# Optimization experiments

Measured on AMD Instinct MI355X. Metric: run time of the kernel, lower is better.

The kernel has to match this reference:

```python
import math
import jax, jax.numpy as jnp
import numpy as np
from jax import lax

B, C, H, W, D = 8, 3, 512, 512, 256
KS, SIGMA = 13, 2.0  # GaussianBlur(13); torchvision samples sigma in (0.1,5.0) -> fixed for determinism


def tanh01(v):
    return jnp.tanh(v) * 0.5 + 0.5


def tanh_range(v, left, right):
    return tanh01(v) * (right - left) + left


def norm01(v):
    return (v - v.min()) / (v.max() - v.min())


def gaussian_blur(x):
    r = KS // 2
    t = jnp.arange(KS, dtype=x.dtype) - r
    k = jnp.exp(-(t ** 2) / (2.0 * SIGMA ** 2))
    k = k / k.sum()
    b, c, h, w = x.shape
    xp = jnp.pad(x, ((0, 0), (0, 0), (r, r), (r, r)), mode='reflect').reshape(b * c, 1, h + 2 * r, w + 2 * r)
    y = lax.conv_general_dilated(xp, k.reshape(1, 1, KS, 1), (1, 1), 'VALID')
    y = lax.conv_general_dilated(y, k.reshape(1, 1, 1, KS), (1, 1), 'VALID')
    return y.reshape(b, c, h, w)


def dark_channel(x):
    return x.min(axis=1, keepdims=True)


def atmospheric_light(x, dark, top_k=1000):
    b, _, h, w = x.shape
    imsz = h * w
    numpx = max(imsz // top_k, 1)
    darkvec = dark.reshape(b, imsz)
    imvec = x.reshape(b, 3, imsz).transpose(0, 2, 1)  # [b, imsz, 3]
    idx = jnp.argsort(darkvec, axis=1)[:, imsz - numpx:]  # brightest dark-channel pixels
    gathered = jnp.take_along_axis(imvec, idx[:, :, None], axis=1)  # [b, numpx, 3]
    a = gathered[:, 1:, :].sum(axis=1) / numpx  # original loop skips index 0 of the slice
    return a[:, :, None, None]  # [b,3,1,1]


def fft_filter(x, rate, fft_gate):
    # rate: [b,1]; replicate torch.fft.fftshift default (shifts ALL axes, incl. batch/channel)
    b, c, w, h = x.shape  # note: original names w,h = shape[-2:]
    line = jnp.floor(jnp.sqrt(w * h * rate) / 2.0).astype(jnp.int32).reshape(-1)  # [b]
    rows = jnp.arange(w)
    cols = jnp.arange(h)
    mr = (rows[None, :] >= w // 2 - line[:, None]) & (rows[None, :] < w // 2 + line[:, None])
    mc = (cols[None, :] >= h // 2 - line[:, None]) & (cols[None, :] < h // 2 + line[:, None])
    mask = (mr[:, None, :, None] & mc[:, None, None, :]).astype(x.dtype)  # [b,1,w,h]
    mask = jnp.broadcast_to(mask, x.shape)
    F = jnp.fft.fftshift(jnp.fft.fft2(x, norm='forward'))
    F = F * (1.0 - mask)
    inv = jnp.fft.ifft2(jnp.fft.ifftshift(F), norm='forward').real
    return jnp.abs(inv) * fft_gate[:, None, None, None]


def setup_inputs() -> dict:
    key = jax.random.key(0)
    ks = jax.random.split(key, 20)
    def lin_w(k, i, o):
        return (jax.random.normal(k, (i, o)) * 0.02).astype(jnp.float32)
    def lin_b(k, o):
        return (jax.random.normal(k, (o,)) * 0.02).astype(jnp.float32)
    return {
        'x': jax.random.uniform(ks[0], (B, C, H, W), dtype=jnp.float32),
        'latent': (jax.random.normal(ks[1], (B, D)) * 0.5).astype(jnp.float32),
        'gate_w': lin_w(ks[2], D, 8), 'gate_b': lin_b(ks[3], 8),
        'wb_w': lin_w(ks[4], D, 3), 'wb_b': lin_b(ks[5], 3),
        'gamma_w': lin_w(ks[6], D, 1), 'gamma_b': lin_b(ks[7], 1),
        'sharp_w': lin_w(ks[8], D, 1), 'sharp_b': lin_b(ks[9], 1),
        'defog_w': lin_w(ks[10], D, 1), 'defog_b': lin_b(ks[11], 1),
        'contrast_w': lin_w(ks[12], D, 1), 'contrast_b': lin_b(ks[13], 1),
        'tone_w': lin_w(ks[14], D, 8), 'tone_b': lin_b(ks[15], 8),
        'fft_w': lin_w(ks[16], D, 1), 'fft_b': lin_b(ks[17], 1),
    }


def reference(x, latent, gate_w, gate_b, wb_w, wb_b, gamma_w, gamma_b, sharp_w, sharp_b,
              defog_w, defog_b, contrast_w, contrast_b, tone_w, tone_b, fft_w, fft_b):
    gate = tanh_range(latent @ gate_w + gate_b, 0.01, 1.0)  # [B,8]

    # white balance
    wb = jnp.exp(tanh_range(latent @ wb_w + wb_b, -0.5, 0.5))
    cs = 1.0 / (1e-5 + 0.27 * wb[:, 0] + 0.67 * wb[:, 1] + 0.06 * wb[:, 2])
    wb = cs[:, None] * wb
    wb_out = norm01(wb[:, :, None, None] * x) * gate[:, 0][:, None, None, None]

    # gamma balance
    lg = math.log(2.5)
    gamma = jnp.exp(tanh_range(latent @ gamma_w + gamma_b, -lg, lg))[:, :, None, None]
    g_out = norm01(jnp.maximum(x, 1e-4) ** gamma) * gate[:, 1][:, None, None, None]

    # identity
    id_out = x * gate[:, 2][:, None, None, None]

    # sharpening
    y = tanh_range(latent @ sharp_w + sharp_b, 0.1, 1.0)[:, :, None, None]
    s = x + y * (x - gaussian_blur(x))
    sharp_out = norm01(s) * gate[:, 3][:, None, None, None]

    # defog (atmospheric scattering model)
    omega = tanh_range(latent @ defog_w + defog_b, 0.1, 1.0)[:, :, None, None]
    dark = dark_channel(x)
    a = atmospheric_light(x, dark)
    t = 1.0 - omega * dark_channel(x / a)
    j = (x - a) / jnp.maximum(t, 0.01) + a
    fog_out = norm01(j) * gate[:, 4][:, None, None, None]

    # contrast
    alpha = jnp.tanh(latent @ contrast_w + contrast_b)[:, :, None, None]
    lum = jnp.clip(0.27 * x[:, 0] + 0.67 * x[:, 1] + 0.06 * x[:, 2], 0.0, 1.0)[:, None]
    clum = -jnp.cos(math.pi * lum) * 0.5 + 0.5
    cimg = x / (lum + 1e-6) * clum
    cimg = (1.0 - alpha) * x + alpha * cimg
    contrast_out = norm01(cimg) * gate[:, 5][:, None, None, None]

    # tone curve (8 fixed segments)
    tc = tanh_range(latent @ tone_w + tone_b, 0.5, 2.0)  # [B,8]
    tsum = tc.sum(axis=1) + 1e-30
    total = jnp.zeros_like(x)
    for i in range(8):
        total = total + jnp.clip(x - i / 8.0, 0.0, 1.0 / 8.0) * tc[:, i][:, None, None, None]
    total = total * (8.0 / tsum)[:, None, None, None]
    tone_out = norm01(total) * gate[:, 6][:, None, None, None]

    # fft frequency masking
    rate = tanh_range(latent @ fft_w + fft_b, 0.1, 0.8)  # [B,1]
    fft_out = fft_filter(x, rate, gate[:, 7])

    return norm01(wb_out + g_out + id_out + sharp_out + fog_out + contrast_out + tone_out + fft_out)
```

## Files before the change

### kernel.cpp

```cpp
#include <hip/hip_runtime.h>
#include <math.h>

#define HW 262144
#define TOTAL 6291456
#define PI_F 3.14159265358979323846f
#define NBIN 1024
#define PIDX(i) ((i) + ((i) >> 3))


#define PF_GATE 0
#define PF_WB 64
#define PF_GAMMA 88
#define PF_Y 96
#define PF_OMEGA 104
#define PF_ALPHA 112
#define PF_TC 120
#define PF_TSC 184
#define PF_RATE 192
#define PF_FG 200
#define PF_A 208
#define PF_WBM 256
#define PF_WBA 264
#define PF_GM 272
#define PF_GA 280
#define PF_SM 288
#define PF_SA 296
#define PF_FM 304
#define PF_FA 312
#define PF_CM 320
#define PF_CA 328
#define PF_TM 336
#define PF_TA 344
#define PF_LINE 360
#define PF_TCS 368
#define PF_TPRE 432
#define PF_IA 496

#define QX(b,c) ((b)*3+(c))
#define QS 24
#define QJ 25
#define QC 26
#define QFIN 27
#define SL_LCOUNT 1792
#define SL_BINSTAR 1920
#define SL_RNEED 1928
#define SL_SUMA2 2048

struct GK { float w[13]; };

__device__ __forceinline__ void waveFence(){ __builtin_amdgcn_wave_barrier(); }

__device__ __forceinline__ unsigned fkey(float f){
    unsigned u = __float_as_uint(f);
    return (u & 0x80000000u) ? ~u : (u | 0x80000000u);
}
__device__ __forceinline__ float funkey(unsigned k){
    return (k & 0x80000000u) ? __uint_as_float(k & 0x7FFFFFFFu) : __uint_as_float(~k);
}

__device__ __forceinline__ void blockRedPair(unsigned kmn, unsigned kmx, int q,
                                             unsigned* slots, unsigned* lds8){
    #pragma unroll
    for (int o = 32; o > 0; o >>= 1){
        kmn = min(kmn, __shfl_down(kmn, o));
        kmx = max(kmx, __shfl_down(kmx, o));
    }
    int w = threadIdx.x >> 6;
    if ((threadIdx.x & 63) == 0){ lds8[w] = kmn; lds8[4+w] = kmx; }
    __syncthreads();
    if (threadIdx.x == 0){
        unsigned mn = min(min(lds8[0],lds8[1]), min(lds8[2],lds8[3]));
        unsigned mx = max(max(lds8[4],lds8[5]), max(lds8[6],lds8[7]));
        int s = blockIdx.x & 31;
        atomicMin(&slots[q*64 + s], mn);
        atomicMax(&slots[q*64 + 32 + s], mx);
    }
    __syncthreads();
}

__device__ __forceinline__ float toneF(float v, const float* tc, float tsc){
    float tn = 0.f;
    #pragma unroll
    for (int i = 0; i < 8; ++i){
        float d = v - 0.125f * (float)i;
        d = fminf(fmaxf(d, 0.f), 0.125f);
        tn += d * tc[i];
    }
    return tn * tsc;
}

__device__ __forceinline__ float2 cadd(float2 a, float2 b){ return make_float2(a.x+b.x, a.y+b.y); }
__device__ __forceinline__ float2 csub(float2 a, float2 b){ return make_float2(a.x-b.x, a.y-b.y); }
__device__ __forceinline__ float2 cmul(float2 a, float2 b){ return make_float2(a.x*b.x - a.y*b.y, a.x*b.y + a.y*b.x); }

template<int S>
__device__ __forceinline__ float2 rot90(float2 z){
    return (S < 0) ? make_float2(z.y, -z.x) : make_float2(-z.y, z.x);
}

template<int S>
__device__ __forceinline__ void fft4p(float2 a, float2 b, float2 c, float2 d,
                                      float2& X0, float2& X1, float2& X2, float2& X3){
    float2 t0 = cadd(a,c), t1 = csub(a,c), t2 = cadd(b,d), t3 = csub(b,d);
    float2 it3 = rot90<S>(t3);
    X0 = cadd(t0,t2); X2 = csub(t0,t2);
    X1 = cadd(t1,it3); X3 = csub(t1,it3);
}

template<int S>
__device__ __forceinline__ void bfly8(float2 v[8]){
    const float C = 0.70710678118654752f;
    float2 E0,E1,E2,E3,O0,O1,O2,O3;
    fft4p<S>(v[0],v[2],v[4],v[6], E0,E1,E2,E3);
    fft4p<S>(v[1],v[3],v[5],v[7], O0,O1,O2,O3);
    float2 w1 = make_float2(C, (S<0) ? -C : C);
    float2 w3 = make_float2(-C, (S<0) ? -C : C);
    float2 u1 = cmul(O1, w1);
    float2 u2 = rot90<S>(O2);
    float2 u3 = cmul(O3, w3);
    v[0]=cadd(E0,O0); v[4]=csub(E0,O0);
    v[1]=cadd(E1,u1); v[5]=csub(E1,u1);
    v[2]=cadd(E2,u2); v[6]=csub(E2,u2);
    v[3]=cadd(E3,u3); v[7]=csub(E3,u3);
}

__device__ __forceinline__ void twiddles(float2 v[8], float th){
    float sn, cs; __sincosf(th, &sn, &cs);
    float2 w1 = make_float2(cs, sn);
    float2 w = w1;
    v[1] = cmul(v[1], w1);
    #pragma unroll
    for (int r = 2; r < 8; ++r){ w = cmul(w, w1); v[r] = cmul(v[r], w); }
}

template<int S>
__device__ __forceinline__ void fft512reg(float2 v[8], float2* buf, int lane){
    bfly8<S>(v);
    #pragma unroll
    for (int q = 0; q < 8; ++q) buf[PIDX(8*lane + q)] = v[q];
    waveFence();
    #pragma unroll
    for (int r = 0; r < 8; ++r) v[r] = buf[PIDX(lane + 64*r)];
    waveFence();
    twiddles(v, (float)S * 6.2831853072f * (float)(lane & 7) * (1.0f/64.0f));
    bfly8<S>(v);
    {
        int basei = ((lane >> 3) << 6) + (lane & 7);
        #pragma unroll
        for (int q = 0; q < 8; ++q) buf[PIDX(basei + 8*q)] = v[q];
    }
    waveFence();
    #pragma unroll
    for (int r = 0; r < 8; ++r) v[r] = buf[PIDX(lane + 64*r)];
    waveFence();
    twiddles(v, (float)S * 6.2831853072f * (float)lane * (1.0f/512.0f));
    bfly8<S>(v);
}

__global__ __launch_bounds__(256) void kSetup(
    const float* __restrict__ lat,
    const float* gw, const float* gb, const float* wbw, const float* wbb,
    const float* gaw, const float* gab, const float* shw, const float* shb,
    const float* dfw, const float* dfb, const float* ctw, const float* ctb,
    const float* tow, const float* tob, const float* ffw, const float* ffb,
    float* P, unsigned* slots, unsigned* hist)
{
    if (blockIdx.x != 0){
        int i = (blockIdx.x - 1) * 256 + threadIdx.x;
        if (i < 4096) slots[i] = (i < 1792 && (i & 63) < 32) ? 0xFFFFFFFFu : 0u;
        if (i < 8192) hist[i] = 0u;
        return;
    }
    int t = threadIdx.x;
    if (t < 192){
        int b = t / 24, o = t % 24;
        const float* L = lat + b * 256;
        const float* W; float bias; int nc, col;
        if (o < 8)      { W=gw;  bias=gb[o];     nc=8; col=o;    }
        else if (o < 11){ W=wbw; bias=wbb[o-8];  nc=3; col=o-8;  }
        else if (o==11) { W=gaw; bias=gab[0];    nc=1; col=0;    }
        else if (o==12) { W=shw; bias=shb[0];    nc=1; col=0;    }
        else if (o==13) { W=dfw; bias=dfb[0];    nc=1; col=0;    }
        else if (o==14) { W=ctw; bias=ctb[0];    nc=1; col=0;    }
        else if (o<23)  { W=tow; bias=tob[o-15]; nc=8; col=o-15; }
        else            { W=ffw; bias=ffb[0];    nc=1; col=0;    }
        float acc = bias;
        for (int d = 0; d < 256; ++d) acc += L[d] * W[d*nc + col];
        float t01 = tanhf(acc) * 0.5f + 0.5f;
        if (o < 8){ float v = t01*0.99f + 0.01f; P[PF_GATE + b*8 + o] = v; if (o==7) P[PF_FG + b] = v; }
        else if (o < 11){ P[PF_WB + b*3 + (o-8)] = expf(t01 - 0.5f); }
        else if (o==11){ float lg = logf(2.5f); P[PF_GAMMA + b] = expf(t01*(2.f*lg) - lg); }
        else if (o==12){ P[PF_Y + b] = t01*0.9f + 0.1f; }
        else if (o==13){ P[PF_OMEGA + b] = t01*0.9f + 0.1f; }
        else if (o==14){ P[PF_ALPHA + b] = tanhf(acc); }
        else if (o<23){ P[PF_TC + b*8 + (o-15)] = t01*1.5f + 0.5f; }
        else { P[PF_RATE + b] = t01*0.7f + 0.1f; }
    }
    __syncthreads();
    if (t < 8){
        int b = t;
        float w0=P[PF_WB+b*3], w1=P[PF_WB+b*3+1], w2=P[PF_WB+b*3+2];
        float cs = 1.0f / (1e-5f + 0.27f*w0 + 0.67f*w1 + 0.06f*w2);
        P[PF_WB+b*3] = cs*w0; P[PF_WB+b*3+1] = cs*w1; P[PF_WB+b*3+2] = cs*w2;
        float ts = 0.f;
        for (int i = 0; i < 8; ++i) ts += P[PF_TC + b*8 + i];
        float tsc = 8.0f / (ts + 1e-30f);
        P[PF_TSC + b] = tsc;
        float acc = 0.f;
        for (int k = 0; k < 8; ++k){
            float tck = P[PF_TC + b*8 + k] * tsc;
            P[PF_TCS + b*8 + k] = tck;
            P[PF_TPRE + b*8 + k] = acc;
            acc += tck * 0.125f;
        }
        int bs = (b + 4) & 7;
        ((int*)(P + PF_LINE))[b] = (int)floorf(sqrtf(262144.0f * P[PF_RATE + bs]) * 0.5f);
    }
}

__global__ __launch_bounds__(256) void kMinmaxHist(const float* __restrict__ x, unsigned* slots, unsigned* hist){
    __shared__ unsigned h[NBIN];
    __shared__ unsigned lds8[8];
    int b = blockIdx.x >> 7;
    int blk = blockIdx.x & 127;
    for (int i = threadIdx.x; i < NBIN; i += 256) h[i] = 0u;
    __syncthreads();
    size_t xb = (size_t)b*3*HW;
    int p0 = (((blk<<1)    )*256 + threadIdx.x) << 2;
    int p1 = (((blk<<1) + 1)*256 + threadIdx.x) << 2;
    float4 u0 = *(const float4*)(x + xb + p0);
    float4 u1 = *(const float4*)(x + xb + HW + p0);
    float4 u2 = *(const float4*)(x + xb + 2*HW + p0);
    float4 w0 = *(const float4*)(x + xb + p1);
    float4 w1 = *(const float4*)(x + xb + HW + p1);
    float4 w2 = *(const float4*)(x + xb + 2*HW + p1);
    float a0[8] = {u0.x,u0.y,u0.z,u0.w, w0.x,w0.y,w0.z,w0.w};
    float a1[8] = {u1.x,u1.y,u1.z,u1.w, w1.x,w1.y,w1.z,w1.w};
    float a2[8] = {u2.x,u2.y,u2.z,u2.w, w2.x,w2.y,w2.z,w2.w};
    float mn0=1e30f,mx0=-1e30f,mn1=1e30f,mx1=-1e30f,mn2=1e30f,mx2=-1e30f;
    #pragma unroll
    for (int e = 0; e < 8; ++e){
        float dark = fminf(a0[e], fminf(a1[e], a2[e]));
        atomicAdd(&h[min(NBIN-1, (int)(dark * (float)NBIN))], 1u);
        mn0 = fminf(mn0, a0[e]); mx0 = fmaxf(mx0, a0[e]);
        mn1 = fminf(mn1, a1[e]); mx1 = fmaxf(mx1, a1[e]);
        mn2 = fminf(mn2, a2[e]); mx2 = fmaxf(mx2, a2[e]);
    }
    __syncthreads();
    for (int i = threadIdx.x; i < NBIN; i += 256){
        unsigned c = h[i];
        if (c) atomicAdd(&hist[b*NBIN + i], c);
    }
    blockRedPair(fkey(mn0), fkey(mx0), QX(b,0), slots, lds8);
    blockRedPair(fkey(mn1), fkey(mx1), QX(b,1), slots, lds8);
    blockRedPair(fkey(mn2), fkey(mx2), QX(b,2), slots, lds8);
}

__global__ __launch_bounds__(256) void kScanHist(const unsigned* __restrict__ hist, unsigned* slots){
    int b = blockIdx.x, t = threadIdx.x;
    __shared__ unsigned wtot[4];
    __shared__ int doneS;
    if (t == 0) doneS = 0;
    __syncthreads();
    unsigned total = 0;
    for (int c0 = 0; c0 < NBIN; c0 += 256){
        int binIdx = NBIN-1 - (c0 + t);
        unsigned cnt = hist[b*NBIN + binIdx];
        unsigned v = cnt;
        #pragma unroll
        for (int off = 1; off < 64; off <<= 1){
            unsigned u = __shfl_up(v, off);
            if ((t & 63) >= off) v += u;
        }
        if ((t & 63) == 63) wtot[t >> 6] = v;
        __syncthreads();
        unsigned wofs = 0;
        for (int w = 0; w < (t >> 6); ++w) wofs += wtot[w];
        unsigned incl = total + wofs + v;
        unsigned excl = incl - cnt;
        if (incl >= 261u && excl < 261u){
            slots[SL_BINSTAR + b] = (unsigned)binIdx;
            slots[SL_RNEED + b]   = 261u - excl;
            doneS = 1;
        }
        __syncthreads();
        if (doneS) break;
        total += wtot[0] + wtot[1] + wtot[2] + wtot[3];
        __syncthreads();
    }
}

__global__ __launch_bounds__(256) void kCollect(const float* __restrict__ x, unsigned* slots, uint2* list){
    __shared__ float wsum[3][4];
    int b = blockIdx.x >> 8;
    int tile = blockIdx.x & 255;
    size_t xb = (size_t)b*3*HW;
    int p = (tile*256 + threadIdx.x) << 2;
    float4 v0 = *(const float4*)(x + xb + p);
    float4 v1 = *(const float4*)(x + xb + HW + p);
    float4 v2 = *(const float4*)(x + xb + 2*HW + p);
    int bs = (int)slots[SL_BINSTAR + b];
    float a0[4] = {v0.x,v0.y,v0.z,v0.w};
    float a1[4] = {v1.x,v1.y,v1.z,v1.w};
    float a2[4] = {v2.x,v2.y,v2.z,v2.w};
    float s0 = 0.f, s1 = 0.f, s2 = 0.f;
    #pragma unroll
    for (int e = 0; e < 4; ++e){
        float dark = fminf(a0[e], fminf(a1[e], a2[e]));
        int bin = min(NBIN-1, (int)(dark * (float)NBIN));
        if (bin > bs){ s0 += a0[e]; s1 += a1[e]; s2 += a2[e]; }
        else if (bin == bs){
            unsigned n = atomicAdd(&slots[SL_LCOUNT + b], 1u);
            if (n < 1024u) list[(b << 10) + n] = make_uint2(__float_as_uint(dark), (unsigned)(p + e));
        }
    }
    #pragma unroll
    for (int o = 32; o > 0; o >>= 1){
        s0 += __shfl_down(s0, o); s1 += __shfl_down(s1, o); s2 += __shfl_down(s2, o);
    }
    int w = threadIdx.x >> 6;
    if ((threadIdx.x & 63) == 0){ wsum[0][w] = s0; wsum[1][w] = s1; wsum[2][w] = s2; }
    __syncthreads();
    if (threadIdx.x == 0){
        float t0 = wsum[0][0]+wsum[0][1]+wsum[0][2]+wsum[0][3];
        float t1 = wsum[1][0]+wsum[1][1]+wsum[1][2]+wsum[1][3];
        float t2 = wsum[2][0]+wsum[2][1]+wsum[2][2]+wsum[2][3];
        float* F = (float*)(slots + SL_SUMA2);
        int sl = blockIdx.x & 31;
        atomicAdd(&F[(b*3+0)*32 + sl], t0);
        atomicAdd(&F[(b*3+1)*32 + sl], t1);
        atomicAdd(&F[(b*3+2)*32 + sl], t2);
    }
}

__global__ void kSelect(const float* __restrict__ x, uint2* list, unsigned* slots, float* P){
    __shared__ unsigned pid[262];
    __shared__ char taken[1024];
    int b = blockIdx.x, t = threadIdx.x;
    int n = (int)min(slots[SL_LCOUNT + b], 1024u);
    int r = (int)slots[SL_RNEED + b];
    if (r > n) r = n;
    const uint2* L = &list[b << 10];
    for (int i = t; i < n; i += 64) taken[i] = 0;
    __syncthreads();
    for (int it = 0; it < r; ++it){
        unsigned long long bk = 0ull; int bp = -1;
        for (int i = t; i < n; i += 64){
            if (taken[i]) continue;
            uint2 e = L[i];
            unsigned long long key = ((unsigned long long)e.x << 32) | e.y;
            if (key > bk){ bk = key; bp = i; }
        }
        #pragma unroll
        for (int o = 32; o > 0; o >>= 1){
            unsigned long long ok = __shfl_down(bk, o);
            int op = __shfl_down(bp, o);
            if (ok > bk){ bk = ok; bp = op; }
        }
        bp = __shfl(bp, 0);
        if (t == 0){ pid[it] = L[bp].y; taken[bp] = 1; }
        __syncthreads();
    }
    float s0 = 0.f, s1 = 0.f, s2 = 0.f;
    size_t xb = (size_t)b*3*HW;
    for (int i = t; i < r; i += 64){
        unsigned id = pid[i];
        s0 += x[xb + id]; s1 += x[xb + HW + id]; s2 += x[xb + 2*HW + id];
    }
    #pragma unroll
    for (int o = 32; o > 0; o >>= 1){
        s0 += __shfl_down(s0, o); s1 += __shfl_down(s1, o); s2 += __shfl_down(s2, o);
    }
    if (t == 0){
        const float* F = (const float*)(slots + SL_SUMA2);
        float f0 = 0.f, f1 = 0.f, f2 = 0.f;
        for (int k = 0; k < 32; ++k){
            f0 += F[(b*3+0)*32 + k];
            f1 += F[(b*3+1)*32 + k];
            f2 += F[(b*3+2)*32 + k];
        }
        float A0 = (s0 + f0) / 262.0f, A1 = (s1 + f1) / 262.0f, A2 = (s2 + f2) / 262.0f;
        P[PF_A + b*3+0] = A0; P[PF_A + b*3+1] = A1; P[PF_A + b*3+2] = A2;
        P[PF_IA + b*3+0] = 1.0f/A0; P[PF_IA + b*3+1] = 1.0f/A1; P[PF_IA + b*3+2] = 1.0f/A2;
    }
}

__global__ __launch_bounds__(256) void kBlur(const float* __restrict__ x, float* __restrict__ blurOut,
                                             const float* __restrict__ P, unsigned* slots, GK gk){
    __shared__ float tile[76][80];
    __shared__ float hbuf[76][68];
    __shared__ unsigned lds8[8];
    int img = blockIdx.x >> 6;
    int tid = blockIdx.x & 63;
    int tr0 = (tid >> 3) << 6;
    int tc0 = (tid & 7) << 6;
    size_t ib = (size_t)img * HW;
    int t = threadIdx.x;
    for (int l = t; l < 76*76; l += 256){
        int r = l / 76, c = l - r*76;
        int gr = tr0 + r - 6; gr = (gr < 0) ? -gr : ((gr > 511) ? 1022 - gr : gr);
        int gc = tc0 + c - 6; gc = (gc < 0) ? -gc : ((gc > 511) ? 1022 - gc : gc);
        tile[r][c] = x[ib + ((size_t)gr << 9) + gc];
    }
    __syncthreads();
    for (int l = t; l < 76*64; l += 256){
        int r = l >> 6, c = l & 63;
        float acc = 0.f;
        #pragma unroll
        for (int k = 0; k < 13; ++k) acc += gk.w[k] * tile[r][c + k];
        hbuf[r][c] = acc;
    }
    __syncthreads();
    float yb = P[PF_Y + img/3];
    unsigned kmn = 0xFFFFFFFFu, kmx = 0u;
    for (int l = t; l < 64*64; l += 256){
        int r = l >> 6, c = l & 63;
        float acc = 0.f;
        #pragma unroll
        for (int k = 0; k < 13; ++k) acc += gk.w[k] * hbuf[r + k][c];
        blurOut[ib + ((size_t)(tr0 + r) << 9) + tc0 + c] = acc;
        float xv = tile[r + 6][c + 6];
        float s = xv + yb * (xv - acc);
        unsigned key = fkey(s);
        kmn = min(kmn, key); kmx = max(kmx, key);
    }
    blockRedPair(kmn, kmx, QS, slots, lds8);
}

__global__ __launch_bounds__(256) void kFftRowFwdJC(const float* __restrict__ x, float2* __restrict__ bc,
                                                    const float* __restrict__ P, unsigned* slots){
    __shared__ float2 buf4[4][580];
    __shared__ unsigned lds8[8];
    float (*xs)[3][512] = reinterpret_cast<float(*)[3][512]>(&buf4[0][0]);
    int b = blockIdx.x >> 8;
    int rp = blockIdx.x & 255;
    int t = threadIdx.x;
    #pragma unroll
    for (int k = 0; k < 3; ++k){
        int l = t + (k << 8);
        int seg = l >> 7;
        int idx = (l & 127) << 2;
        int ch = seg >> 1, rr = seg & 1;
        float4 z = *(const float4*)(x + (size_t)(3*b + ch)*HW + ((size_t)(2*rp + rr) << 9) + idx);
        *(float4*)&xs[rr][ch][idx] = z;
    }
    __syncthreads();
    {
        float ia0 = P[PF_IA+b*3], ia1 = P[PF_IA+b*3+1], ia2 = P[PF_IA+b*3+2];
        float a0 = P[PF_A+b*3],  a1 = P[PF_A+b*3+1],  a2 = P[PF_A+b*3+2];
        float om = P[PF_OMEGA+b], al = P[PF_ALPHA+b];
        int rr = t >> 7, c4 = (t & 127) << 2;
        float4 xv0 = *(float4*)&xs[rr][0][c4];
        float4 xv1 = *(float4*)&xs[rr][1][c4];
        float4 xv2 = *(float4*)&xs[rr][2][c4];
        float A0[4]={xv0.x,xv0.y,xv0.z,xv0.w}, A1[4]={xv1.x,xv1.y,xv1.z,xv1.w}, A2[4]={xv2.x,xv2.y,xv2.z,xv2.w};
        float jmn = 1e30f, jmx = -1e30f, cmn = 1e30f, cmx = -1e30f;
        #pragma unroll
        for (int e = 0; e < 4; ++e){
            float x0 = A0[e], x1 = A1[e], x2 = A2[e];
            float dr = fminf(x0*ia0, fminf(x1*ia1, x2*ia2));
            float T = fmaxf(1.0f - om*dr, 0.01f);
            float rT = 1.0f / T;
            float j0 = (x0-a0)*rT + a0, j1 = (x1-a1)*rT + a1, j2 = (x2-a2)*rT + a2;
            float lum = fminf(fmaxf(0.27f*x0 + 0.67f*x1 + 0.06f*x2, 0.f), 1.f);
            float clum = -__cosf(PI_F*lum)*0.5f + 0.5f;
            float alx = (1.f - al) + al * (clum / (lum + 1e-6f));
            float c0 = x0*alx, c1 = x1*alx, c2 = x2*alx;
            jmn = fminf(jmn, fminf(j0, fminf(j1, j2))); jmx = fmaxf(jmx, fmaxf(j0, fmaxf(j1, j2)));
            cmn = fminf(cmn, fminf(c0, fminf(c1, c2))); cmx = fmaxf(cmx, fmaxf(c0, fmaxf(c1, c2)));
        }
        blockRedPair(fkey(jmn), fkey(jmx), QJ, slots, lds8);
        blockRedPair(fkey(cmn), fkey(cmx), QC, slots, lds8);
    }
    int u = t >> 6, lane = t & 63;
    int frr = u >> 1, pk = u & 1;
    float2 v[8];
    #pragma unroll
    for (int r = 0; r < 8; ++r){
        int i = lane + 64*r;
        if (pk == 0) v[r] = make_float2(xs[frr][0][i] * (1.0f/512.0f), xs[frr][1][i] * (1.0f/512.0f));
        else         v[r] = make_float2(xs[frr][2][i] * (1.0f/512.0f), 0.f);
    }
    __syncthreads();
    fft512reg<-1>(v, buf4[u], lane);
    size_t ob = (size_t)(2*b + pk)*HW + ((size_t)(2*rp + frr) << 9);
    #pragma unroll
    for (int q = 0; q < 8; ++q) bc[ob + lane + 64*q] = v[q];
}

__global__ __launch_bounds__(256) void kFftColMid(float2* __restrict__ bc, const int* __restrict__ lineS){
    int img  = blockIdx.x >> 6;
    int tile = blockIdx.x & 63;
    int c0 = tile << 3;
    int line = lineS[img >> 1];
    if (c0 >= line && c0 + 8 <= 512 - line) return;
    __shared__ float2 cb[8][580];
    int t = threadIdx.x;
    size_t ibase = (size_t)img*HW + c0;
    for (int k = 0; k < 16; ++k){
        int idx = (k << 8) + t;
        int row = idx >> 3, col = idx & 7;
        float2 z = bc[ibase + ((size_t)row << 9) + col];
        cb[col][PIDX(row)] = make_float2(z.x * (1.0f/512.0f), z.y * (1.0f/512.0f));
    }
    __syncthreads();
    int lane = t & 63, u = t >> 6;
    #pragma unroll
    for (int h = 0; h < 2; ++h){
        int col = (h << 2) + u;
        int cc = c0 + col;
        bool colM = (cc < line) || (cc >= 512 - line);
        float2 v[8];
        #pragma unroll
        for (int r = 0; r < 8; ++r) v[r] = cb[col][PIDX(lane + 64*r)];
        waveFence();
        fft512reg<-1>(v, cb[col], lane);
        if (colM){
            #pragma unroll
            for (int q = 0; q < 8; ++q){
                int f = lane + (q << 6);
                if (f < line || f >= 512 - line) v[q] = make_float2(0.f, 0.f);
            }
        }
        waveFence();
        fft512reg<+1>(v, cb[col], lane);
        #pragma unroll
        for (int q = 0; q < 8; ++q) cb[col][PIDX(lane + 64*q)] = v[q];
        waveFence();
    }
    __syncthreads();
    for (int k = 0; k < 16; ++k){
        int idx = (k << 8) + t;
        int row = idx >> 3, col = idx & 7;
        int cc = c0 + col;
        if (cc < line || cc >= 512 - line)
            bc[ibase + ((size_t)row << 9) + col] = cb[col][PIDX(row)];
    }
}

__global__ __launch_bounds__(256) void kCombineFFT(const float* __restrict__ x, float* __restrict__ outb,
                                                   const float2* __restrict__ bc, const float* __restrict__ P,
                                                   unsigned* slots){
    __shared__ float2 buf4[4][580];
    __shared__ float stc[8], spre[8];
    __shared__ unsigned lds8[8];
    float (*fbuf)[3][512] = reinterpret_cast<float(*)[3][512]>(&buf4[0][0]);
    int b = blockIdx.x >> 8;
    int rp = blockIdx.x & 255;
    int t = threadIdx.x;
    if (t < 8){ stc[t] = P[PF_TCS + b*8 + t]; spre[t] = P[PF_TPRE + b*8 + t]; }
    int u = t >> 6, lane = t & 63;
    int frr = u >> 1, pk = u & 1;
    float2 v[8];
    size_t ib = (size_t)(2*b + pk)*HW + ((size_t)(2*rp + frr) << 9);
    #pragma unroll
    for (int r = 0; r < 8; ++r) v[r] = bc[ib + lane + 64*r];
    fft512reg<+1>(v, buf4[u], lane);
    __syncthreads();
    if (pk == 0){
        #pragma unroll
        for (int q = 0; q < 8; ++q){
            int i = lane + 64*q;
            fbuf[frr][0][i] = fabsf(v[q].x);
            fbuf[frr][1][i] = fabsf(v[q].y);
        }
    } else {
        #pragma unroll
        for (int q = 0; q < 8; ++q) fbuf[frr][2][lane + 64*q] = fabsf(v[q].x);
    }
    __syncthreads();

    float g  = P[PF_FG + b];
    float wb0=P[PF_WB+b*3], wb1=P[PF_WB+b*3+1], wb2=P[PF_WB+b*3+2];
    float gam=P[PF_GAMMA+b], yb=P[PF_Y+b], om=P[PF_OMEGA+b], al=P[PF_ALPHA+b];
    float a0=P[PF_A+b*3], a1=P[PF_A+b*3+1], a2=P[PF_A+b*3+2];
    float ia0=P[PF_IA+b*3], ia1=P[PF_IA+b*3+1], ia2=P[PF_IA+b*3+2];
    float g2=P[PF_GATE+b*8+2];
    float wbm=P[PF_WBM+b], wba=P[PF_WBA+b], gm=P[PF_GM+b], ga=P[PF_GA+b];
    float sm=P[PF_SM+b], sa=P[PF_SA+b], fm=P[PF_FM+b], fa=P[PF_FA+b];
    float cm=P[PF_CM+b], ca=P[PF_CA+b], tm=P[PF_TM+b], ta=P[PF_TA+b];
    float kadd = wba + ga + sa + fa + ca + ta;

    int rr = t >> 7, c4 = (t & 127) << 2;
    size_t p0 = (size_t)(3*b)*HW + ((size_t)(2*rp + rr) << 9) + c4;
    float4 xv0 = *(const float4*)(x + p0);
    float4 xv1 = *(const float4*)(x + p0 + HW);
    float4 xv2 = *(const float4*)(x + p0 + 2*HW);
    float4 bv0 = *(const float4*)(outb + p0);
    float4 bv1 = *(const float4*)(outb + p0 + HW);
    float4 bv2 = *(const float4*)(outb + p0 + 2*HW);
    float4 fv0 = *(float4*)&fbuf[rr][0][c4];
    float4 fv1 = *(float4*)&fbuf[rr][1][c4];
    float4 fv2 = *(float4*)&fbuf[rr][2][c4];
    float X0[4]={xv0.x,xv0.y,xv0.z,xv0.w}, X1[4]={xv1.x,xv1.y,xv1.z,xv1.w}, X2[4]={xv2.x,xv2.y,xv2.z,xv2.w};
    float B0[4]={bv0.x,bv0.y,bv0.z,bv0.w}, B1[4]={bv1.x,bv1.y,bv1.z,bv1.w}, B2[4]={bv2.x,bv2.y,bv2.z,bv2.w};
    float F0[4]={fv0.x,fv0.y,fv0.z,fv0.w}, F1[4]={fv1.x,fv1.y,fv1.z,fv1.w}, F2[4]={fv2.x,fv2.y,fv2.z,fv2.w};
    float O0[4], O1[4], O2[4];
    float mn = 1e30f, mx = -1e30f;
    #pragma unroll
    for (int e = 0; e < 4; ++e){
        float x0 = X0[e], x1 = X1[e], x2 = X2[e];
        float dr = fminf(x0*ia0, fminf(x1*ia1, x2*ia2));
        float T = fmaxf(1.0f - om*dr, 0.01f);
        float rT = 1.0f / T;
        float lum = fminf(fmaxf(0.27f*x0 + 0.67f*x1 + 0.06f*x2, 0.f), 1.f);
        float clum = -__cosf(PI_F*lum)*0.5f + 0.5f;
        float alx = (1.f - al) + al * (clum / (lum + 1e-6f));
        #pragma unroll
        for (int ch = 0; ch < 3; ++ch){
            float xv = (ch==0)?x0:((ch==1)?x1:x2);
            float bl = (ch==0)?B0[e]:((ch==1)?B1[e]:B2[e]);
            float fv = (ch==0)?F0[e]:((ch==1)?F1[e]:F2[e]);
            float wb = (ch==0)?wb0:((ch==1)?wb1:wb2);
            float av = (ch==0)?a0:((ch==1)?a1:a2);
            float s = xv + yb*(xv - bl);
            float j = (xv - av)*rT + av;
            float ci = xv * alx;
            int k = min(7, (int)(xv * 8.0f));
            float tn = spre[k] + (xv - 0.125f*(float)k) * stc[k];
            float gp = __powf(fmaxf(xv, 1e-4f), gam);
            float sum = (wb*xv)*wbm + gp*gm + xv*g2 + s*sm + j*fm + ci*cm + tn*tm + kadd + fv*g;
            if (ch==0) O0[e]=sum; else if (ch==1) O1[e]=sum; else O2[e]=sum;
            mn = fminf(mn, sum); mx = fmaxf(mx, sum);
        }
    }
    *(float4*)(outb + p0)        = make_float4(O0[0],O0[1],O0[2],O0[3]);
    *(float4*)(outb + p0 + HW)   = make_float4(O1[0],O1[1],O1[2],O1[3]);
    *(float4*)(outb + p0 + 2*HW) = make_float4(O2[0],O2[1],O2[2],O2[3]);
    blockRedPair(fkey(mn), fkey(mx), QFIN, slots, lds8);
}

__global__ void kNormParams(float* P, const unsigned* __restrict__ slots){
    __shared__ float mnv[28], mxv[28];
    int t = threadIdx.x;
    if (t < 28){
        unsigned kmn = 0xFFFFFFFFu, kmx = 0u;
        for (int s = 0; s < 32; ++s){
            kmn = min(kmn, slots[t*64 + s]);
            kmx = max(kmx, slots[t*64 + 32 + s]);
        }
        mnv[t] = funkey(kmn); mxv[t] = funkey(kmx);
    }
    __syncthreads();
    if (t == 0){
        float wmin=1e30f, wmax=-1e30f, gmin=1e30f, gmax=-1e30f, tmin=1e30f, tmax=-1e30f;
        for (int b = 0; b < 8; ++b){
            float gam = P[PF_GAMMA+b];
            float tsc = P[PF_TSC+b];
            const float* tc = &P[PF_TC + b*8];
            float xbmin = 1e30f, xbmax = -1e30f;
            for (int c = 0; c < 3; ++c){
                int i = b*3 + c;
                float w = P[PF_WB + i];
                wmin = fminf(wmin, w * mnv[i]); wmax = fmaxf(wmax, w * mxv[i]);
                gmin = fminf(gmin, __powf(fmaxf(mnv[i], 1e-4f), gam));
                gmax = fmaxf(gmax, __powf(fmaxf(mxv[i], 1e-4f), gam));
                xbmin = fminf(xbmin, mnv[i]); xbmax = fmaxf(xbmax, mxv[i]);
            }
            tmin = fminf(tmin, toneF(xbmin, tc, tsc));
            tmax = fmaxf(tmax, toneF(xbmax, tc, tsc));
        }
        float smin = mnv[QS], smax = mxv[QS];
        float jmin = mnv[QJ], jmax = mxv[QJ];
        float cmin = mnv[QC], cmax = mxv[QC];
        for (int b = 0; b < 8; ++b){
            const float* G = &P[PF_GATE + b*8];
            float m;
            m = G[0]/(wmax-wmin); P[PF_WBM+b]=m; P[PF_WBA+b]=-wmin*m;
            m = G[1]/(gmax-gmin); P[PF_GM +b]=m; P[PF_GA +b]=-gmin*m;
            m = G[3]/(smax-smin); P[PF_SM +b]=m; P[PF_SA +b]=-smin*m;
            m = G[4]/(jmax-jmin); P[PF_FM +b]=m; P[PF_FA +b]=-jmin*m;
            m = G[5]/(cmax-cmin); P[PF_CM +b]=m; P[PF_CA +b]=-cmin*m;
            m = G[6]/(tmax-tmin); P[PF_TM +b]=m; P[PF_TA +b]=-tmin*m;
        }
    }
}

__global__ __launch_bounds__(256) void kFinalNorm(float* __restrict__ out, const unsigned* __restrict__ slots){
    unsigned kmn = 0xFFFFFFFFu, kmx = 0u;
    for (int s = 0; s < 32; ++s){
        kmn = min(kmn, slots[QFIN*64 + s]);
        kmx = max(kmx, slots[QFIN*64 + 32 + s]);
    }
    float mn = funkey(kmn), mx = funkey(kmx);
    float inv = 1.0f / (mx - mn);
    size_t i = ((size_t)blockIdx.x*256 + threadIdx.x) << 2;
    float4 v = *(const float4*)(out + i);
    v.x = (v.x - mn) * inv; v.y = (v.y - mn) * inv;
    v.z = (v.z - mn) * inv; v.w = (v.w - mn) * inv;
    *(float4*)(out + i) = v;
}

extern "C" void kernel_launch(void* const* d_in, const int* in_sizes, int n_in,
                              void* d_out, int out_size, void* d_ws, size_t ws_size,
                              hipStream_t stream){
    const float* x   = (const float*)d_in[0];
    const float* lat = (const float*)d_in[1];
    const float* gw  = (const float*)d_in[2];  const float* gb  = (const float*)d_in[3];
    const float* wbw = (const float*)d_in[4];  const float* wbb = (const float*)d_in[5];
    const float* gaw = (const float*)d_in[6];  const float* gab = (const float*)d_in[7];
    const float* shw = (const float*)d_in[8];  const float* shb = (const float*)d_in[9];
    const float* dfw = (const float*)d_in[10]; const float* dfb = (const float*)d_in[11];
    const float* ctw = (const float*)d_in[12]; const float* ctb = (const float*)d_in[13];
    const float* tow = (const float*)d_in[14]; const float* tob = (const float*)d_in[15];
    const float* ffw = (const float*)d_in[16]; const float* ffb = (const float*)d_in[17];
    float* out = (float*)d_out;
    char* ws = (char*)d_ws;

    float*    P     = (float*)ws;
    unsigned* slots = (unsigned*)(ws + 4096);
    unsigned* hist  = (unsigned*)(ws + 20480);
    uint2*    list  = (uint2*)(ws + 540672);
    float2*   bufC  = (float2*)(ws + 1048576);
    const int* lineS = (const int*)(P + PF_LINE);

    GK gk;
    {
        float s = 0.f;
        for (int i = 0; i < 13; ++i){ float t = (float)i - 6.f; gk.w[i] = expf(-(t*t)/8.0f); s += gk.w[i]; }
        for (int i = 0; i < 13; ++i) gk.w[i] /= s;
    }

    hipLaunchKernelGGL(kSetup,       dim3(41),   dim3(256), 0, stream, lat, gw,gb,wbw,wbb,gaw,gab,shw,shb,dfw,dfb,ctw,ctb,tow,tob,ffw,ffb, P, slots, hist);
    hipLaunchKernelGGL(kMinmaxHist,  dim3(1024), dim3(256), 0, stream, x, slots, hist);
    hipLaunchKernelGGL(kScanHist,    dim3(8),    dim3(256), 0, stream, hist, slots);
    hipLaunchKernelGGL(kCollect,     dim3(2048), dim3(256), 0, stream, x, slots, list);
    hipLaunchKernelGGL(kSelect,      dim3(8),    dim3(64),  0, stream, x, list, slots, P);
    hipLaunchKernelGGL(kBlur,        dim3(1536), dim3(256), 0, stream, x, out, P, slots, gk);
    hipLaunchKernelGGL(kFftRowFwdJC, dim3(2048), dim3(256), 0, stream, x, bufC, P, slots);
    hipLaunchKernelGGL(kFftColMid,   dim3(1024), dim3(256), 0, stream, bufC, lineS);
    hipLaunchKernelGGL(kNormParams,  dim3(1),    dim3(64),  0, stream, P, slots);
    hipLaunchKernelGGL(kCombineFFT,  dim3(2048), dim3(256), 0, stream, x, out, bufC, P, slots);
    hipLaunchKernelGGL(kFinalNorm,   dim3(6144), dim3(256), 0, stream, out, slots);
}
```

Measured before the change: 199.4 us.

## Pack two real channel-2 rows per complex FFT and split spectra after transform

The row FFT kernels now process four rows per block with six waves. Channels 0 and 1 are packed into one complex FFT per row, and channel 2 of two adjacent rows shares one complex FFT. The two real spectra are separated with the conjugate-symmetry trick, so five of the previous six 512-point FFTs per row pair's worth of work become fewer transforms. The inverse kernel recombines the channel-2 pair before a single inverse FFT. This adds an LDS round trip and a separation step, and changes the block shape to 384 threads with 1024 blocks.

Result: slower. 212.3 us (+6.5%).

```diff
diff --git a/kernel.cpp b/kernel.cpp
--- a/kernel.cpp
+++ b/kernel.cpp
@@ -58,19 +58,19 @@
     return (k & 0x80000000u) ? __uint_as_float(k & 0x7FFFFFFFu) : __uint_as_float(~k);
 }
 
-__device__ __forceinline__ void blockRedPair(unsigned kmn, unsigned kmx, int q,
-                                             unsigned* slots, unsigned* lds8){
+__device__ __forceinline__ void blockRedPairN(unsigned kmn, unsigned kmx, int q,
+                                              unsigned* slots, unsigned* ldsw, int nw){
     #pragma unroll
     for (int o = 32; o > 0; o >>= 1){
         kmn = min(kmn, __shfl_down(kmn, o));
         kmx = max(kmx, __shfl_down(kmx, o));
     }
     int w = threadIdx.x >> 6;
-    if ((threadIdx.x & 63) == 0){ lds8[w] = kmn; lds8[4+w] = kmx; }
+    if ((threadIdx.x & 63) == 0){ ldsw[w] = kmn; ldsw[nw + w] = kmx; }
     __syncthreads();
     if (threadIdx.x == 0){
-        unsigned mn = min(min(lds8[0],lds8[1]), min(lds8[2],lds8[3]));
-        unsigned mx = max(max(lds8[4],lds8[5]), max(lds8[6],lds8[7]));
+        unsigned mn = ldsw[0], mx = ldsw[nw];
+        for (int i = 1; i < nw; ++i){ mn = min(mn, ldsw[i]); mx = max(mx, ldsw[nw+i]); }
         int s = blockIdx.x & 31;
         atomicMin(&slots[q*64 + s], mn);
         atomicMax(&slots[q*64 + 32 + s], mx);
@@ -251,9 +251,9 @@
         unsigned c = h[i];
         if (c) atomicAdd(&hist[b*NBIN + i], c);
     }
-    blockRedPair(fkey(mn0), fkey(mx0), QX(b,0), slots, lds8);
-    blockRedPair(fkey(mn1), fkey(mx1), QX(b,1), slots, lds8);
-    blockRedPair(fkey(mn2), fkey(mx2), QX(b,2), slots, lds8);
+    blockRedPairN(fkey(mn0), fkey(mx0), QX(b,0), slots, lds8, 4);
+    blockRedPairN(fkey(mn1), fkey(mx1), QX(b,1), slots, lds8, 4);
+    blockRedPairN(fkey(mn2), fkey(mx2), QX(b,2), slots, lds8, 4);
 }
 
 __global__ __launch_bounds__(256) void kScanHist(const unsigned* __restrict__ hist, unsigned* slots){
@@ -424,68 +424,97 @@
         unsigned key = fkey(s);
         kmn = min(kmn, key); kmx = max(kmx, key);
     }
-    blockRedPair(kmn, kmx, QS, slots, lds8);
-}
-
-__global__ __launch_bounds__(256) void kFftRowFwdJC(const float* __restrict__ x, float2* __restrict__ bc,
+    blockRedPairN(kmn, kmx, QS, slots, lds8, 4);
+}
+
+__global__ __launch_bounds__(384) void kFftRowFwdJC(const float* __restrict__ x, float2* __restrict__ bc,
                                                     const float* __restrict__ P, unsigned* slots){
-    __shared__ float2 buf4[4][580];
-    __shared__ unsigned lds8[8];
-    float (*xs)[3][512] = reinterpret_cast<float(*)[3][512]>(&buf4[0][0]);
-    int b = blockIdx.x >> 8;
-    int rp = blockIdx.x & 255;
+    __shared__ float2 buf6[6][580];
+    __shared__ unsigned lds12[12];
+    float (*xs)[3][512] = reinterpret_cast<float(*)[3][512]>(&buf6[0][0]);
+    int b = blockIdx.x >> 7;
+    int rq = blockIdx.x & 127;
     int t = threadIdx.x;
     #pragma unroll
-    for (int k = 0; k < 3; ++k){
-        int l = t + (k << 8);
-        int seg = l >> 7;
+    for (int k = 0; k < 4; ++k){
+        int l = t + k*384;
+        int rc = l >> 7;
         int idx = (l & 127) << 2;
-        int ch = seg >> 1, rr = seg & 1;
-        float4 z = *(const float4*)(x + (size_t)(3*b + ch)*HW + ((size_t)(2*rp + rr) << 9) + idx);
-        *(float4*)&xs[rr][ch][idx] = z;
+        int row = rc / 3, ch = rc - row*3;
+        float4 z = *(const float4*)(x + (size_t)(3*b + ch)*HW + ((size_t)(4*rq + row) << 9) + idx);
+        *(float4*)&xs[row][ch][idx] = z;
     }
     __syncthreads();
     {
         float ia0 = P[PF_IA+b*3], ia1 = P[PF_IA+b*3+1], ia2 = P[PF_IA+b*3+2];
         float a0 = P[PF_A+b*3],  a1 = P[PF_A+b*3+1],  a2 = P[PF_A+b*3+2];
         float om = P[PF_OMEGA+b], al = P[PF_ALPHA+b];
-        int rr = t >> 7, c4 = (t & 127) << 2;
-        float4 xv0 = *(float4*)&xs[rr][0][c4];
-        float4 xv1 = *(float4*)&xs[rr][1][c4];
-        float4 xv2 = *(float4*)&xs[rr][2][c4];
-        float A0[4]={xv0.x,xv0.y,xv0.z,xv0.w}, A1[4]={xv1.x,xv1.y,xv1.z,xv1.w}, A2[4]={xv2.x,xv2.y,xv2.z,xv2.w};
         float jmn = 1e30f, jmx = -1e30f, cmn = 1e30f, cmx = -1e30f;
-        #pragma unroll
-        for (int e = 0; e < 4; ++e){
-            float x0 = A0[e], x1 = A1[e], x2 = A2[e];
-            float dr = fminf(x0*ia0, fminf(x1*ia1, x2*ia2));
-            float T = fmaxf(1.0f - om*dr, 0.01f);
-            float rT = 1.0f / T;
-            float j0 = (x0-a0)*rT + a0, j1 = (x1-a1)*rT + a1, j2 = (x2-a2)*rT + a2;
-            float lum = fminf(fmaxf(0.27f*x0 + 0.67f*x1 + 0.06f*x2, 0.f), 1.f);
-            float clum = -__cosf(PI_F*lum)*0.5f + 0.5f;
-            float alx = (1.f - al) + al * (clum / (lum + 1e-6f));
-            float c0 = x0*alx, c1 = x1*alx, c2 = x2*alx;
-            jmn = fminf(jmn, fminf(j0, fminf(j1, j2))); jmx = fmaxf(jmx, fmaxf(j0, fmaxf(j1, j2)));
-            cmn = fminf(cmn, fminf(c0, fminf(c1, c2))); cmx = fmaxf(cmx, fmaxf(c0, fmaxf(c1, c2)));
-        }
-        blockRedPair(fkey(jmn), fkey(jmx), QJ, slots, lds8);
-        blockRedPair(fkey(cmn), fkey(cmx), QC, slots, lds8);
+        for (int it = 0; it < 2; ++it){
+            int g = t + it*384;
+            if (g >= 512) break;
+            int row = g >> 7, c4 = (g & 127) << 2;
+            float4 xv0 = *(float4*)&xs[row][0][c4];
+            float4 xv1 = *(float4*)&xs[row][1][c4];
+            float4 xv2 = *(float4*)&xs[row][2][c4];
+            float A0[4]={xv0.x,xv0.y,xv0.z,xv0.w}, A1[4]={xv1.x,xv1.y,xv1.z,xv1.w}, A2[4]={xv2.x,xv2.y,xv2.z,xv2.w};
+            #pragma unroll
+            for (int e = 0; e < 4; ++e){
+                float x0 = A0[e], x1 = A1[e], x2 = A2[e];
+                float dr = fminf(x0*ia0, fminf(x1*ia1, x2*ia2));
+                float T = fmaxf(1.0f - om*dr, 0.01f);
+                float rT = 1.0f / T;
+                float j0 = (x0-a0)*rT + a0, j1 = (x1-a1)*rT + a1, j2 = (x2-a2)*rT + a2;
+                float lum = fminf(fmaxf(0.27f*x0 + 0.67f*x1 + 0.06f*x2, 0.f), 1.f);
+                float clum = -__cosf(PI_F*lum)*0.5f + 0.5f;
+                float alx = (1.f - al) + al * (clum / (lum + 1e-6f));
+                float c0 = x0*alx, c1 = x1*alx, c2 = x2*alx;
+                jmn = fminf(jmn, fminf(j0, fminf(j1, j2))); jmx = fmaxf(jmx, fmaxf(j0, fmaxf(j1, j2)));
+                cmn = fminf(cmn, fminf(c0, fminf(c1, c2))); cmx = fmaxf(cmx, fmaxf(c0, fmaxf(c1, c2)));
+            }
+        }
+        blockRedPairN(fkey(jmn), fkey(jmx), QJ, slots, lds12, 6);
+        blockRedPairN(fkey(cmn), fkey(cmx), QC, slots, lds12, 6);
     }
     int u = t >> 6, lane = t & 63;
-    int frr = u >> 1, pk = u & 1;
     float2 v[8];
-    #pragma unroll
-    for (int r = 0; r < 8; ++r){
-        int i = lane + 64*r;
-        if (pk == 0) v[r] = make_float2(xs[frr][0][i] * (1.0f/512.0f), xs[frr][1][i] * (1.0f/512.0f));
-        else         v[r] = make_float2(xs[frr][2][i] * (1.0f/512.0f), 0.f);
-    }
-    __syncthreads();
-    fft512reg<-1>(v, buf4[u], lane);
-    size_t ob = (size_t)(2*b + pk)*HW + ((size_t)(2*rp + frr) << 9);
-    #pragma unroll
-    for (int q = 0; q < 8; ++q) bc[ob + lane + 64*q] = v[q];
+    if (u < 4){
+        #pragma unroll
+        for (int r = 0; r < 8; ++r){
+            int i = lane + 64*r;
+            v[r] = make_float2(xs[u][0][i] * (1.0f/512.0f), xs[u][1][i] * (1.0f/512.0f));
+        }
+    } else {
+        int pr = (u - 4) * 2;
+        #pragma unroll
+        for (int r = 0; r < 8; ++r){
+            int i = lane + 64*r;
+            v[r] = make_float2(xs[pr][2][i] * (1.0f/512.0f), xs[pr+1][2][i] * (1.0f/512.0f));
+        }
+    }
+    __syncthreads();
+    fft512reg<-1>(v, buf6[u], lane);
+    if (u < 4){
+        size_t ob = (size_t)(2*b)*HW + ((size_t)(4*rq + u) << 9);
+        #pragma unroll
+        for (int q = 0; q < 8; ++q) bc[ob + lane + 64*q] = v[q];
+    } else {
+        float2* B = buf6[u];
+        #pragma unroll
+        for (int q = 0; q < 8; ++q) B[PIDX(lane + 64*q)] = v[q];
+        waveFence();
+        int pr = (u - 4) * 2;
+        size_t o0 = (size_t)(2*b+1)*HW + ((size_t)(4*rq + pr) << 9);
+        size_t o1 = o0 + 512;
+        #pragma unroll
+        for (int q = 0; q < 8; ++q){
+            int f = lane + 64*q;
+            float2 Z = v[q];
+            float2 M = B[PIDX((512 - f) & 511)];
+            bc[o0 + f] = make_float2(0.5f*(Z.x + M.x),  0.5f*(Z.y - M.y));
+            bc[o1 + f] = make_float2(0.5f*(Z.y + M.y), -0.5f*(Z.x - M.x));
+        }
+    }
 }
 
 __global__ __launch_bounds__(256) void kFftColMid(float2* __restrict__ bc, const int* __restrict__ lineS){
@@ -538,35 +567,51 @@
     }
 }
 
-__global__ __launch_bounds__(256) void kCombineFFT(const float* __restrict__ x, float* __restrict__ outb,
+__global__ __launch_bounds__(384) void kCombineFFT(const float* __restrict__ x, float* __restrict__ outb,
                                                    const float2* __restrict__ bc, const float* __restrict__ P,
                                                    unsigned* slots){
-    __shared__ float2 buf4[4][580];
+    __shared__ float2 buf6[6][580];
     __shared__ float stc[8], spre[8];
-    __shared__ unsigned lds8[8];
-    float (*fbuf)[3][512] = reinterpret_cast<float(*)[3][512]>(&buf4[0][0]);
-    int b = blockIdx.x >> 8;
-    int rp = blockIdx.x & 255;
+    __shared__ unsigned lds12[12];
+    float (*fbuf)[3][512] = reinterpret_cast<float(*)[3][512]>(&buf6[0][0]);
+    int b = blockIdx.x >> 7;
+    int rq = blockIdx.x & 127;
     int t = threadIdx.x;
     if (t < 8){ stc[t] = P[PF_TCS + b*8 + t]; spre[t] = P[PF_TPRE + b*8 + t]; }
     int u = t >> 6, lane = t & 63;
-    int frr = u >> 1, pk = u & 1;
     float2 v[8];
-    size_t ib = (size_t)(2*b + pk)*HW + ((size_t)(2*rp + frr) << 9);
-    #pragma unroll
-    for (int r = 0; r < 8; ++r) v[r] = bc[ib + lane + 64*r];
-    fft512reg<+1>(v, buf4[u], lane);
-    __syncthreads();
-    if (pk == 0){
+    if (u < 4){
+        size_t ib = (size_t)(2*b)*HW + ((size_t)(4*rq + u) << 9);
+        #pragma unroll
+        for (int r = 0; r < 8; ++r) v[r] = bc[ib + lane + 64*r];
+    } else {
+        int pr = (u - 4) * 2;
+        size_t i0 = (size_t)(2*b+1)*HW + ((size_t)(4*rq + pr) << 9);
+        #pragma unroll
+        for (int r = 0; r < 8; ++r){
+            int i = lane + 64*r;
+            float2 s0 = bc[i0 + i];
+            float2 s1 = bc[i0 + 512 + i];
+            v[r] = make_float2(s0.x - s1.y, s0.y + s1.x);
+        }
+    }
+    fft512reg<+1>(v, buf6[u], lane);
+    __syncthreads();
+    if (u < 4){
         #pragma unroll
         for (int q = 0; q < 8; ++q){
             int i = lane + 64*q;
-            fbuf[frr][0][i] = fabsf(v[q].x);
-            fbuf[frr][1][i] = fabsf(v[q].y);
+            fbuf[u][0][i] = fabsf(v[q].x);
+            fbuf[u][1][i] = fabsf(v[q].y);
         }
     } else {
-        #pragma unroll
-        for (int q = 0; q < 8; ++q) fbuf[frr][2][lane + 64*q] = fabsf(v[q].x);
+        int pr = (u - 4) * 2;
+        #pragma unroll
+        for (int q = 0; q < 8; ++q){
+            int i = lane + 64*q;
+            fbuf[pr][2][i]   = fabsf(v[q].x);
+            fbuf[pr+1][2][i] = fabsf(v[q].y);
+        }
     }
     __syncthreads();
 
@@ -581,53 +626,57 @@
     float cm=P[PF_CM+b], ca=P[PF_CA+b], tm=P[PF_TM+b], ta=P[PF_TA+b];
     float kadd = wba + ga + sa + fa + ca + ta;
 
-    int rr = t >> 7, c4 = (t & 127) << 2;
-    size_t p0 = (size_t)(3*b)*HW + ((size_t)(2*rp + rr) << 9) + c4;
-    float4 xv0 = *(const float4*)(x + p0);
-    float4 xv1 = *(const float4*)(x + p0 + HW);
-    float4 xv2 = *(const float4*)(x + p0 + 2*HW);
-    float4 bv0 = *(const float4*)(outb + p0);
-    float4 bv1 = *(const float4*)(outb + p0 + HW);
-    float4 bv2 = *(const float4*)(outb + p0 + 2*HW);
-    float4 fv0 = *(float4*)&fbuf[rr][0][c4];
-    float4 fv1 = *(float4*)&fbuf[rr][1][c4];
-    float4 fv2 = *(float4*)&fbuf[rr][2][c4];
-    float X0[4]={xv0.x,xv0.y,xv0.z,xv0.w}, X1[4]={xv1.x,xv1.y,xv1.z,xv1.w}, X2[4]={xv2.x,xv2.y,xv2.z,xv2.w};
-    float B0[4]={bv0.x,bv0.y,bv0.z,bv0.w}, B1[4]={bv1.x,bv1.y,bv1.z,bv1.w}, B2[4]={bv2.x,bv2.y,bv2.z,bv2.w};
-    float F0[4]={fv0.x,fv0.y,fv0.z,fv0.w}, F1[4]={fv1.x,fv1.y,fv1.z,fv1.w}, F2[4]={fv2.x,fv2.y,fv2.z,fv2.w};
-    float O0[4], O1[4], O2[4];
     float mn = 1e30f, mx = -1e30f;
-    #pragma unroll
-    for (int e = 0; e < 4; ++e){
-        float x0 = X0[e], x1 = X1[e], x2 = X2[e];
-        float dr = fminf(x0*ia0, fminf(x1*ia1, x2*ia2));
-        float T = fmaxf(1.0f - om*dr, 0.01f);
-        float rT = 1.0f / T;
-        float lum = fminf(fmaxf(0.27f*x0 + 0.67f*x1 + 0.06f*x2, 0.f), 1.f);
-        float clum = -__cosf(PI_F*lum)*0.5f + 0.5f;
-        float alx = (1.f - al) + al * (clum / (lum + 1e-6f));
-        #pragma unroll
-        for (int ch = 0; ch < 3; ++ch){
-            float xv = (ch==0)?x0:((ch==1)?x1:x2);
-            float bl = (ch==0)?B0[e]:((ch==1)?B1[e]:B2[e]);
-            float fv = (ch==0)?F0[e]:((ch==1)?F1[e]:F2[e]);
-            float wb = (ch==0)?wb0:((ch==1)?wb1:wb2);
-            float av = (ch==0)?a0:((ch==1)?a1:a2);
-            float s = xv + yb*(xv - bl);
-            float j = (xv - av)*rT + av;
-            float ci = xv * alx;
-            int k = min(7, (int)(xv * 8.0f));
-            float tn = spre[k] + (xv - 0.125f*(float)k) * stc[k];
-            float gp = __powf(fmaxf(xv, 1e-4f), gam);
-            float sum = (wb*xv)*wbm + gp*gm + xv*g2 + s*sm + j*fm + ci*cm + tn*tm + kadd + fv*g;
-            if (ch==0) O0[e]=sum; else if (ch==1) O1[e]=sum; else O2[e]=sum;
-            mn = fminf(mn, sum); mx = fmaxf(mx, sum);
-        }
-    }
-    *(float4*)(outb + p0)        = make_float4(O0[0],O0[1],O0[2],O0[3]);
-    *(float4*)(outb + p0 + HW)   = make_float4(O1[0],O1[1],O1[2],O1[3]);
-    *(float4*)(outb + p0 + 2*HW) = make_float4(O2[0],O2[1],O2[2],O2[3]);
-    blockRedPair(fkey(mn), fkey(mx), QFIN, slots, lds8);
+    for (int it = 0; it < 2; ++it){
+        int gidx = t + it*384;
+        if (gidx >= 512) break;
+        int row = gidx >> 7, c4 = (gidx & 127) << 2;
+        size_t p0 = (size_t)(3*b)*HW + ((size_t)(4*rq + row) << 9) + c4;
+        float4 xv0 = *(const float4*)(x + p0);
+        float4 xv1 = *(const float4*)(x + p0 + HW);
+        float4 xv2 = *(const float4*)(x + p0 + 2*HW);
+        float4 bv0 = *(const float4*)(outb + p0);
+        float4 bv1 = *(const float4*)(outb + p0 + HW);
+        float4 bv2 = *(const float4*)(outb + p0 + 2*HW);
+        float4 fv0 = *(float4*)&fbuf[row][0][c4];
+        float4 fv1 = *(float4*)&fbuf[row][1][c4];
+        float4 fv2 = *(float4*)&fbuf[row][2][c4];
+        float X0[4]={xv0.x,xv0.y,xv0.z,xv0.w}, X1[4]={xv1.x,xv1.y,xv1.z,xv1.w}, X2[4]={xv2.x,xv2.y,xv2.z,xv2.w};
+        float B0[4]={bv0.x,bv0.y,bv0.z,bv0.w}, B1[4]={bv1.x,bv1.y,bv1.z,bv1.w}, B2[4]={bv2.x,bv2.y,bv2.z,bv2.w};
+        float F0[4]={fv0.x,fv0.y,fv0.z,fv0.w}, F1[4]={fv1.x,fv1.y,fv1.z,fv1.w}, F2[4]={fv2.x,fv2.y,fv2.z,fv2.w};
+        float O0[4], O1[4], O2[4];
+        #pragma unroll
+        for (int e = 0; e < 4; ++e){
+            float x0 = X0[e], x1 = X1[e], x2 = X2[e];
+            float dr = fminf(x0*ia0, fminf(x1*ia1, x2*ia2));
+            float T = fmaxf(1.0f - om*dr, 0.01f);
+            float rT = 1.0f / T;
+            float lum = fminf(fmaxf(0.27f*x0 + 0.67f*x1 + 0.06f*x2, 0.f), 1.f);
+            float clum = -__cosf(PI_F*lum)*0.5f + 0.5f;
+            float alx = (1.f - al) + al * (clum / (lum + 1e-6f));
+            #pragma unroll
+            for (int ch = 0; ch < 3; ++ch){
+                float xv = (ch==0)?x0:((ch==1)?x1:x2);
+                float bl = (ch==0)?B0[e]:((ch==1)?B1[e]:B2[e]);
+                float fv = (ch==0)?F0[e]:((ch==1)?F1[e]:F2[e]);
+                float wb = (ch==0)?wb0:((ch==1)?wb1:wb2);
+                float av = (ch==0)?a0:((ch==1)?a1:a2);
+                float s = xv + yb*(xv - bl);
+                float j = (xv - av)*rT + av;
+                float ci = xv * alx;
+                int k = min(7, (int)(xv * 8.0f));
+                float tn = spre[k] + (xv - 0.125f*(float)k) * stc[k];
+                float gp = __powf(fmaxf(xv, 1e-4f), gam);
+                float sum = (wb*xv)*wbm + gp*gm + xv*g2 + s*sm + j*fm + ci*cm + tn*tm + kadd + fv*g;
+                if (ch==0) O0[e]=sum; else if (ch==1) O1[e]=sum; else O2[e]=sum;
+                mn = fminf(mn, sum); mx = fmaxf(mx, sum);
+            }
+        }
+        *(float4*)(outb + p0)        = make_float4(O0[0],O0[1],O0[2],O0[3]);
+        *(float4*)(outb + p0 + HW)   = make_float4(O1[0],O1[1],O1[2],O1[3]);
+        *(float4*)(outb + p0 + 2*HW) = make_float4(O2[0],O2[1],O2[2],O2[3]);
+    }
+    blockRedPairN(fkey(mn), fkey(mx), QFIN, slots, lds12, 6);
 }
 
 __global__ void kNormParams(float* P, const unsigned* __restrict__ slots){
@@ -727,9 +776,9 @@
     hipLaunchKernelGGL(kCollect,     dim3(2048), dim3(256), 0, stream, x, slots, list);
     hipLaunchKernelGGL(kSelect,      dim3(8),    dim3(64),  0, stream, x, list, slots, P);
     hipLaunchKernelGGL(kBlur,        dim3(1536), dim3(256), 0, stream, x, out, P, slots, gk);
-    hipLaunchKernelGGL(kFftRowFwdJC, dim3(2048), dim3(256), 0, stream, x, bufC, P, slots);
+    hipLaunchKernelGGL(kFftRowFwdJC, dim3(1024), dim3(384), 0, stream, x, bufC, P, slots);
     hipLaunchKernelGGL(kFftColMid,   dim3(1024), dim3(256), 0, stream, bufC, lineS);
     hipLaunchKernelGGL(kNormParams,  dim3(1),    dim3(64),  0, stream, P, slots);
-    hipLaunchKernelGGL(kCombineFFT,  dim3(2048), dim3(256), 0, stream, x, out, bufC, P, slots);
+    hipLaunchKernelGGL(kCombineFFT,  dim3(1024), dim3(384), 0, stream, x, out, bufC, P, slots);
     hipLaunchKernelGGL(kFinalNorm,   dim3(6144), dim3(256), 0, stream, out, slots);
 }
```
